# Kernel tuning notes

Hardware: AMD Instinct MI355X
Metric: run time of the kernel (lower is better)

The kernel has to match this reference:

```python
import jax, jax.numpy as jnp
import numpy as np

LAMBDA = 1.0


def _sq_dists(x, y):
    # x: (B,N,3), y: (B,M,3) -> (B,N,M) squared euclidean distances
    x2 = jnp.sum(x * x, axis=-1)  # (B,N)
    y2 = jnp.sum(y * y, axis=-1)  # (B,M)
    xy = jnp.einsum('bnd,bmd->bnm', x, y)  # (B,N,M)
    return x2[:, :, None] + y2[:, None, :] - 2.0 * xy


def setup_inputs() -> dict:
    key = jax.random.key(0)
    k1, k2, k3 = jax.random.split(key, 3)
    B, N = 4, 8192
    pc_pred = jax.random.normal(k1, (B, N, 3), dtype=jnp.float32)
    pc_target = jax.random.normal(k2, (B, N, 3), dtype=jnp.float32)
    fbpp = jax.random.uniform(k3, (1,), dtype=jnp.float32)
    return {"pc_pred": pc_pred, "pc_target": pc_target, "fbpp": fbpp}


def reference(pc_pred, pc_target, fbpp):
    # Chamfer distance (pytorch3d semantics): squared L2 1-NN both directions,
    # mean over points, mean over batch, summed over the two directions.
    d2 = _sq_dists(pc_pred, pc_target)  # (B,N,M)
    cham_x = jnp.mean(jnp.min(d2, axis=2), axis=1)  # (B,) pred -> target
    cham_y = jnp.mean(jnp.min(d2, axis=1), axis=1)  # (B,) target -> pred
    dist = jnp.mean(cham_x) + jnp.mean(cham_y)
    rate = jnp.mean(fbpp)
    loss = dist + LAMBDA * rate
    return (loss, dist, rate)
```

## Files before the change

kernel.cpp:

```cpp
#include <hip/hip_runtime.h>
#include <math.h>

typedef _Float16 f16x8 __attribute__((ext_vector_type(8)));
typedef __fp16   fp16v2 __attribute__((ext_vector_type(2)));
typedef float    f32x16 __attribute__((ext_vector_type(16)));

#define THREADS 256
#define YCHUNK  4096
#define XPB     128

static __device__ inline unsigned pk2(float a, float b) {
    fp16v2 h = __builtin_amdgcn_cvt_pkrtz(a, b);
    return __builtin_bit_cast(unsigned, h);
}

static __device__ inline void packwrite(uint2* dst, float4 f0, float4 f1,
                                        float4 f2) {
    float n0 = fmaf(f0.x, f0.x, fmaf(f0.y, f0.y, f0.z * f0.z));
    float n1 = fmaf(f0.w, f0.w, fmaf(f1.x, f1.x, f1.y * f1.y));
    float n2 = fmaf(f1.z, f1.z, fmaf(f1.w, f1.w, f2.x * f2.x));
    float n3 = fmaf(f2.y, f2.y, fmaf(f2.z, f2.z, f2.w * f2.w));
    dst[0] = make_uint2(pk2(f0.x, f0.y), pk2(f0.z, n0));
    dst[1] = make_uint2(pk2(f0.w, f1.x), pk2(f1.y, n1));
    dst[2] = make_uint2(pk2(f1.z, f1.w), pk2(f2.x, n2));
    dst[3] = make_uint2(pk2(f2.y, f2.z), pk2(f2.w, n3));
}

__global__ __launch_bounds__(THREADS, 2) void chamfer_kernel(
    const float* __restrict__ pred, const float* __restrict__ targ,
    float* __restrict__ partials, int N)
{
    const int dir = blockIdx.z;
    const float* xsrc = dir == 0 ? pred : targ;
    const float* ysrc = dir == 0 ? targ : pred;
    const int b = blockIdx.y;

    __shared__ uint2 sy0[YCHUNK];
    __shared__ uint2 sy1[YCHUNK];
    __shared__ float swave[4];

    const int tid  = threadIdx.x;
    const int lane = tid & 63;
    const int wave = tid >> 6;
    const int col  = lane & 31;

    const size_t xi = (size_t)(b * N + blockIdx.x * XPB + wave * 32 + col) * 3;
    const float x0 = xsrc[xi], x1 = xsrc[xi + 1], x2 = xsrc[xi + 2];

    const bool act = lane < 32;
    f16x8 bf;
    bf[0] = act ? (_Float16)(-2.0f * x0) : (_Float16)0.0f;
    bf[1] = act ? (_Float16)(-2.0f * x1) : (_Float16)0.0f;
    bf[2] = act ? (_Float16)(-2.0f * x2) : (_Float16)0.0f;
    bf[3] = act ? (_Float16)1.0f : (_Float16)0.0f;
    bf[4] = bf[5] = bf[6] = bf[7] = (_Float16)0.0f;

    f32x16 zacc;
    f32x16 vmin;
#pragma unroll
    for (int r = 0; r < 16; ++r) { zacc[r] = 0.0f; vmin[r] = INFINITY; }

    const float4* yf4 = (const float4*)(ysrc + (size_t)b * N * 3);

#pragma unroll
    for (int k = 0; k < 4; ++k) {
        const int fb = k * THREADS * 3 + tid * 3;
        packwrite(&sy0[(k * THREADS + tid) * 4], yf4[fb], yf4[fb + 1],
                  yf4[fb + 2]);
    }

#define GDECL(k)                                                           \
    float4 g##k##a = yf4[3072 + k * THREADS * 3 + tid * 3 + 0];            \
    float4 g##k##b = yf4[3072 + k * THREADS * 3 + tid * 3 + 1];            \
    float4 g##k##c = yf4[3072 + k * THREADS * 3 + tid * 3 + 2]
    GDECL(0); GDECL(1); GDECL(2); GDECL(3);
#undef GDECL

    __syncthreads();

#define LOADJ(j, SY) uint2 lo##j = SY[(i + j) * 32 + col]
#define MFJ(j)                                                             \
    f32x16 ac##j = __builtin_amdgcn_mfma_f32_32x32x16_f16(                 \
        __builtin_bit_cast(f16x8,                                          \
            make_uint4(lo##j.x, lo##j.y, 0u, 0u)), bf, zacc, 0, 0, 0)
#define COMPUTE(SY)                                                        \
    for (int i = 0; i < YCHUNK / 32; i += 8) {                             \
        LOADJ(0, SY); LOADJ(1, SY); LOADJ(2, SY); LOADJ(3, SY);            \
        LOADJ(4, SY); LOADJ(5, SY); LOADJ(6, SY); LOADJ(7, SY);            \
        MFJ(0); MFJ(1); MFJ(2); MFJ(3);                                    \
        MFJ(4); MFJ(5); MFJ(6); MFJ(7);                                    \
        _Pragma("unroll")                                                  \
        for (int r = 0; r < 16; ++r) {                                     \
            vmin[r] = fminf(fminf(vmin[r], ac0[r]), ac1[r]);               \
            vmin[r] = fminf(fminf(vmin[r], ac2[r]), ac3[r]);               \
            vmin[r] = fminf(fminf(vmin[r], ac4[r]), ac5[r]);               \
            vmin[r] = fminf(fminf(vmin[r], ac6[r]), ac7[r]);               \
        }                                                                  \
    }

    COMPUTE(sy0)

    packwrite(&sy1[(0 * THREADS + tid) * 4], g0a, g0b, g0c);
    packwrite(&sy1[(1 * THREADS + tid) * 4], g1a, g1b, g1c);
    packwrite(&sy1[(2 * THREADS + tid) * 4], g2a, g2b, g2c);
    packwrite(&sy1[(3 * THREADS + tid) * 4], g3a, g3b, g3c);
    __syncthreads();

    COMPUTE(sy1)
#undef COMPUTE
#undef LOADJ
#undef MFJ

    float v = vmin[0];
#pragma unroll
    for (int r = 1; r < 16; ++r) v = fminf(v, vmin[r]);
    v = fminf(v, __shfl_xor(v, 32));
    float d = v + fmaf(x0, x0, fmaf(x1, x1, x2 * x2));

#pragma unroll
    for (int off = 16; off > 0; off >>= 1) d += __shfl_xor(d, off);
    if (lane == 0) swave[wave] = d;
    __syncthreads();
    if (tid == 0) {
        float s = swave[0] + swave[1] + swave[2] + swave[3];
        int bid = blockIdx.x + gridDim.x * (blockIdx.y + gridDim.y * blockIdx.z);
        partials[bid] = s;
    }
}

__global__ __launch_bounds__(512) void finalize(
    const float* __restrict__ partials, const float* __restrict__ fbpp,
    float* __restrict__ out, int nPartials, int totalPts)
{
    __shared__ float sw[8];
    const int tid = threadIdx.x;
    float v = (tid < nPartials) ? partials[tid] : 0.0f;
#pragma unroll
    for (int off = 32; off > 0; off >>= 1) v += __shfl_xor(v, off);
    if ((tid & 63) == 0) sw[tid >> 6] = v;
    __syncthreads();
    if (tid == 0) {
        float t = 0.0f;
#pragma unroll
        for (int w = 0; w < 8; ++w) t += sw[w];
        float dist = t / (float)totalPts;
        float rate = fbpp[0];
        out[0] = dist + rate;
        out[1] = dist;
        out[2] = rate;
    }
}

extern "C" void kernel_launch(void* const* d_in, const int* in_sizes, int n_in,
                              void* d_out, int out_size, void* d_ws, size_t ws_size,
                              hipStream_t stream) {
    const float* pred = (const float*)d_in[0];
    const float* targ = (const float*)d_in[1];
    const float* fbpp = (const float*)d_in[2];
    float* out = (float*)d_out;

    const int B = 4;
    const int N = in_sizes[0] / (B * 3);
    float* partials = (float*)d_ws;

    dim3 grid(N / XPB, B, 2);
    chamfer_kernel<<<grid, THREADS, 0, stream>>>(pred, targ, partials, N);

    const int nPartials = (N / XPB) * B * 2;
    finalize<<<1, 512, 0, stream>>>(partials, fbpp, out, nPartials, B * N);
}
```

Before: 24.52 us.

## Software-pipeline MFMA with min3 folding over a single looped LDS chunk

Replaces the two fixed LDS buffers and the prefetch-in-registers scheme with a single 4096-point LDS buffer that is refilled in a loop over N/YCHUNK chunks. The inner loop is software-pipelined so the MFMAs for the next pair of rows are issued while the previous pair's results are folded into the running minimum. The fold uses inline v_min3_f32 to cut the instruction count. Halving LDS use may allow more resident blocks. In exchange, the global loads for the next chunk no longer overlap the compute, since each chunk is loaded between barriers.

```diff
diff --git a/kernel.cpp b/kernel.cpp
--- a/kernel.cpp
+++ b/kernel.cpp
@@ -35,8 +35,7 @@
     const float* ysrc = dir == 0 ? targ : pred;
     const int b = blockIdx.y;
 
-    __shared__ uint2 sy0[YCHUNK];
-    __shared__ uint2 sy1[YCHUNK];
+    __shared__ uint2 sy[YCHUNK];
     __shared__ float swave[4];
 
     const int tid  = threadIdx.x;
@@ -60,56 +59,60 @@
 #pragma unroll
     for (int r = 0; r < 16; ++r) { zacc[r] = 0.0f; vmin[r] = INFINITY; }
 
-    const float4* yf4 = (const float4*)(ysrc + (size_t)b * N * 3);
+#define MF(X)                                                              \
+    __builtin_amdgcn_mfma_f32_32x32x16_f16(                                \
+        __builtin_bit_cast(f16x8, make_uint4((X).x, (X).y, 0u, 0u)),       \
+        bf, zacc, 0, 0, 0)
 
-#pragma unroll
-    for (int k = 0; k < 4; ++k) {
-        const int fb = k * THREADS * 3 + tid * 3;
-        packwrite(&sy0[(k * THREADS + tid) * 4], yf4[fb], yf4[fb + 1],
-                  yf4[fb + 2]);
-    }
-
-#define GDECL(k)                                                           \
-    float4 g##k##a = yf4[3072 + k * THREADS * 3 + tid * 3 + 0];            \
-    float4 g##k##b = yf4[3072 + k * THREADS * 3 + tid * 3 + 1];            \
-    float4 g##k##c = yf4[3072 + k * THREADS * 3 + tid * 3 + 2]
-    GDECL(0); GDECL(1); GDECL(2); GDECL(3);
-#undef GDECL
-
-    __syncthreads();
-
-#define LOADJ(j, SY) uint2 lo##j = SY[(i + j) * 32 + col]
-#define MFJ(j)                                                             \
-    f32x16 ac##j = __builtin_amdgcn_mfma_f32_32x32x16_f16(                 \
-        __builtin_bit_cast(f16x8,                                          \
-            make_uint4(lo##j.x, lo##j.y, 0u, 0u)), bf, zacc, 0, 0, 0)
-#define COMPUTE(SY)                                                        \
-    for (int i = 0; i < YCHUNK / 32; i += 8) {                             \
-        LOADJ(0, SY); LOADJ(1, SY); LOADJ(2, SY); LOADJ(3, SY);            \
-        LOADJ(4, SY); LOADJ(5, SY); LOADJ(6, SY); LOADJ(7, SY);            \
-        MFJ(0); MFJ(1); MFJ(2); MFJ(3);                                    \
-        MFJ(4); MFJ(5); MFJ(6); MFJ(7);                                    \
+#define FOLD(A0, A1)                                                       \
+    {                                                                      \
         _Pragma("unroll")                                                  \
         for (int r = 0; r < 16; ++r) {                                     \
-            vmin[r] = fminf(fminf(vmin[r], ac0[r]), ac1[r]);               \
-            vmin[r] = fminf(fminf(vmin[r], ac2[r]), ac3[r]);               \
-            vmin[r] = fminf(fminf(vmin[r], ac4[r]), ac5[r]);               \
-            vmin[r] = fminf(fminf(vmin[r], ac6[r]), ac7[r]);               \
+            float t_;                                                      \
+            asm("v_min3_f32 %0, %1, %2, %3"                                \
+                : "=v"(t_)                                                 \
+                : "v"(vmin[r]), "v"((A0)[r]), "v"((A1)[r]));               \
+            vmin[r] = t_;                                                  \
         }                                                                  \
     }
 
-    COMPUTE(sy0)
+    const int nchunks = N / YCHUNK;
+    for (int c = 0; c < nchunks; ++c) {
+        __syncthreads();
+        {
+            const float4* yf4 = (const float4*)(ysrc + (size_t)b * N * 3
+                                                + (size_t)c * YCHUNK * 3);
+#pragma unroll
+            for (int k = 0; k < 4; ++k) {
+                const int fb = k * THREADS * 3 + tid * 3;
+                packwrite(&sy[(k * THREADS + tid) * 4], yf4[fb], yf4[fb + 1],
+                          yf4[fb + 2]);
+            }
+        }
+        __syncthreads();
 
-    packwrite(&sy1[(0 * THREADS + tid) * 4], g0a, g0b, g0c);
-    packwrite(&sy1[(1 * THREADS + tid) * 4], g1a, g1b, g1c);
-    packwrite(&sy1[(2 * THREADS + tid) * 4], g2a, g2b, g2c);
-    packwrite(&sy1[(3 * THREADS + tid) * 4], g3a, g3b, g3c);
-    __syncthreads();
-
-    COMPUTE(sy1)
-#undef COMPUTE
-#undef LOADJ
-#undef MFJ
+        uint2 la0 = sy[0 * 32 + col], la1 = sy[1 * 32 + col];
+        f32x16 aa0 = MF(la0), aa1 = MF(la1);
+        for (int g = 2; g <= 122; g += 4) {
+            uint2 lb0 = sy[(g + 0) * 32 + col];
+            uint2 lb1 = sy[(g + 1) * 32 + col];
+            f32x16 ab0 = MF(lb0), ab1 = MF(lb1);
+            FOLD(aa0, aa1);
+            uint2 lc0 = sy[(g + 2) * 32 + col];
+            uint2 lc1 = sy[(g + 3) * 32 + col];
+            aa0 = MF(lc0); aa1 = MF(lc1);
+            FOLD(ab0, ab1);
+        }
+        {
+            uint2 lb0 = sy[126 * 32 + col];
+            uint2 lb1 = sy[127 * 32 + col];
+            f32x16 ab0 = MF(lb0), ab1 = MF(lb1);
+            FOLD(aa0, aa1);
+            FOLD(ab0, ab1);
+        }
+    }
+#undef MF
+#undef FOLD
 
     float v = vmin[0];
 #pragma unroll
```

Measured after the change: 24.93 us. Within noise of the previous version (+1.6%).
